# Kernel optimization log

Measured on AMD Instinct MI355X. Metric: run time of the kernel, lower is better.

## Reference

```python
import jax, jax.numpy as jnp
import numpy as np

N_NODES = 50000
N_EDGES = 600000
N_GRAPHS = 256
IN_C = 128
HID = 128
OUT_C = 2


def setup_inputs() -> dict:
    key = jax.random.key(0)
    ks = jax.random.split(key, 16)
    d = {}
    d["x"] = jax.random.normal(ks[0], (N_NODES, IN_C), jnp.float32)
    d["edge_index"] = jax.random.randint(ks[1], (2, N_EDGES), 0, N_NODES, dtype=jnp.int32)
    d["root_node_idx"] = jax.random.randint(ks[2], (N_GRAPHS,), 0, N_NODES, dtype=jnp.int32)
    d["batch"] = jnp.sort(jax.random.randint(ks[3], (N_NODES,), 0, N_GRAPHS, dtype=jnp.int32))
    dims = [(IN_C, HID), (HID, HID), (HID, HID), (HID, HID)]
    for i, (ci, co) in enumerate(dims, start=1):
        s = 1.0 / np.sqrt(ci)
        d[f"w{i}_l"] = jax.random.uniform(ks[3 + i], (co, ci), jnp.float32, -s, s)
        d[f"b{i}_l"] = jnp.zeros((co,), jnp.float32)
        d[f"w{i}_r"] = jax.random.uniform(ks[7 + i], (co, ci), jnp.float32, -s, s)
    s = 1.0 / np.sqrt(2 * HID)
    d["w_cls"] = jax.random.uniform(ks[12], (OUT_C, 2 * HID), jnp.float32, -s, s)
    d["b_cls"] = jnp.zeros((OUT_C,), jnp.float32)
    return d


def _sage_conv(x, src, tgt, deg_inv, w_l, b_l, w_r):
    # mean aggregation of source features at target nodes (PyG SAGEConv, aggr='mean')
    agg = jax.ops.segment_sum(x[src], tgt, num_segments=N_NODES) * deg_inv  # [N, C]
    # out = lin_l(agg) + lin_r(x); lin_r has no bias in PyG SAGEConv
    return agg @ w_l.T + b_l + x @ w_r.T


def reference(x, edge_index, root_node_idx, batch,
              w1_l, b1_l, w1_r, w2_l, b2_l, w2_r,
              w3_l, b3_l, w3_r, w4_l, b4_l, w4_r,
              w_cls, b_cls):
    src, tgt = edge_index[0], edge_index[1]
    ones_e = jnp.ones((src.shape[0],), x.dtype)
    deg = jax.ops.segment_sum(ones_e, tgt, num_segments=N_NODES)
    deg_inv = (1.0 / jnp.maximum(deg, 1.0))[:, None]  # [N, 1]

    h = jax.nn.relu(_sage_conv(x, src, tgt, deg_inv, w1_l, b1_l, w1_r))
    h = jax.nn.relu(_sage_conv(h, src, tgt, deg_inv, w2_l, b2_l, w2_r))
    h = jax.nn.relu(_sage_conv(h, src, tgt, deg_inv, w3_l, b3_l, w3_r))
    h = jax.nn.relu(_sage_conv(h, src, tgt, deg_inv, w4_l, b4_l, w4_r))

    root_emb = h[root_node_idx]  # [G, HID]
    g_sum = jax.ops.segment_sum(h, batch, num_segments=N_GRAPHS)
    g_cnt = jax.ops.segment_sum(jnp.ones((h.shape[0],), h.dtype), batch, num_segments=N_GRAPHS)
    graph_emb = g_sum / jnp.maximum(g_cnt, 1.0)[:, None]  # [G, HID]

    combined = jnp.concatenate([root_emb, graph_emb], axis=1)  # [G, 2*HID]
    return combined @ w_cls.T + b_cls  # [G, OUT_C]
```

## Files before the change

kernel.cpp:

```cpp
#include <hip/hip_runtime.h>
#include <hip/hip_bf16.h>

#define N_NODES 50000
#define N_EDGES 600000
#define N_GRAPHS 256
#define C 128
#define NB 196
#define PB_DEG 2344
#define PB_XS  6250
#define PB_WS  512

typedef unsigned short ushort;
typedef unsigned int uint;
typedef __attribute__((ext_vector_type(8))) short bfrag8;
typedef __attribute__((ext_vector_type(4))) float facc4;

__device__ __forceinline__ ushort f2bf(float v) {
    uint u = __float_as_uint(v);
    u += 0x7FFFu + ((u >> 16) & 1u);
    return (ushort)(u >> 16);
}
__device__ __forceinline__ float bf2f(ushort u) {
    return __uint_as_float(((uint)u) << 16);
}
__device__ __forceinline__ void fsplit(float v, ushort& h, ushort& l) {
    h = f2bf(v);
    l = f2bf(v - bf2f(h));
}

struct WPtrs { const float* wl[4]; const float* wr[4]; };

__global__ __launch_bounds__(256) void k_prep(const int* __restrict__ tgt,
                                              int* __restrict__ deg,
                                              const float* __restrict__ x,
                                              ushort* __restrict__ Ahi,
                                              ushort* __restrict__ Alo,
                                              WPtrs wp,
                                              ushort* __restrict__ BTh,
                                              ushort* __restrict__ BTl,
                                              const int* __restrict__ batch,
                                              int* __restrict__ gstart) {
    const int b = blockIdx.x, t = threadIdx.x;
    if (b < PB_DEG) {
        int e = b * 256 + t;
        if (e < N_EDGES) atomicAdd(&deg[tgt[e]], 1);
    } else if (b < PB_DEG + PB_XS) {
        int gid = (b - PB_DEG) * 256 + t;
        int n = gid >> 5, c4 = (gid & 31) << 2;
        float4 v = *(const float4*)(x + (size_t)n * C + c4);
        ushort4 h, l;
        fsplit(v.x, h.x, l.x); fsplit(v.y, h.y, l.y);
        fsplit(v.z, h.z, l.z); fsplit(v.w, h.w, l.w);
        *(ushort4*)(Ahi + (size_t)n * 256 + 128 + c4) = h;
        *(ushort4*)(Alo + (size_t)n * 256 + 128 + c4) = l;
    } else if (b < PB_DEG + PB_XS + PB_WS) {
        int gid = (b - PB_DEG - PB_XS) * 256 + t;
        int l = gid >> 15;
        int rem = gid & 32767;
        int n = rem >> 8, k = rem & 255;
        float v = (k < 128) ? wp.wl[l][n * 128 + k] : wp.wr[l][n * 128 + (k - 128)];
        ushort h, lo;
        fsplit(v, h, lo);
        BTh[gid] = h;
        BTl[gid] = lo;
    } else {
        int g = t;
        int lo = 0, hi = N_NODES;
        while (lo < hi) {
            int mid = (lo + hi) >> 1;
            if (batch[mid] < g) lo = mid + 1;
            else hi = mid;
        }
        gstart[g] = lo;
        if (t == 0) gstart[N_GRAPHS] = N_NODES;
    }
}

__global__ __launch_bounds__(256) void k_scan1(const int* __restrict__ deg,
                                               int* __restrict__ bsum,
                                               float* __restrict__ dinv) {
    __shared__ int ws[4];
    int idx = blockIdx.x * 256 + threadIdx.x;
    int v = (idx < N_NODES) ? deg[idx] : 0;
    if (idx < N_NODES) dinv[idx] = 1.0f / fmaxf((float)v, 1.0f);
    int s = v;
#pragma unroll
    for (int off = 1; off < 64; off <<= 1) s += __shfl_xor(s, off);
    if ((threadIdx.x & 63) == 0) ws[threadIdx.x >> 6] = s;
    __syncthreads();
    if (threadIdx.x == 0) bsum[blockIdx.x] = ws[0] + ws[1] + ws[2] + ws[3];
}

__global__ __launch_bounds__(256) void k_scan2(const int* __restrict__ deg,
                                               const int* __restrict__ bsum,
                                               int* __restrict__ rowptr) {
    __shared__ int red[4];
    __shared__ int ws[4];
    const int b = blockIdx.x, t = threadIdx.x;
    const int lane = t & 63, w = t >> 6;
    int bv = (t < NB && t < b) ? bsum[t] : 0;
#pragma unroll
    for (int off = 1; off < 64; off <<= 1) bv += __shfl_xor(bv, off);
    if (lane == 0) red[w] = bv;
    __syncthreads();
    const int boff = red[0] + red[1] + red[2] + red[3];
    int idx = b * 256 + t;
    int v = (idx < N_NODES) ? deg[idx] : 0;
    int incl = v;
#pragma unroll
    for (int off = 1; off < 64; off <<= 1) {
        int u = __shfl_up(incl, off);
        if (lane >= off) incl += u;
    }
    if (lane == 63) ws[w] = incl;
    __syncthreads();
    int wo = 0;
    if (w > 0) wo += ws[0];
    if (w > 1) wo += ws[1];
    if (w > 2) wo += ws[2];
    if (idx < N_NODES) rowptr[idx] = boff + wo + incl - v;
    if (b == 0 && t == 0) rowptr[N_NODES] = N_EDGES;
}

__global__ void k_fill(const int* __restrict__ src, const int* __restrict__ tgt,
                       const int* __restrict__ rowptr, int* __restrict__ fill,
                       int* __restrict__ csr_src) {
    int e = blockIdx.x * blockDim.x + threadIdx.x;
    if (e >= N_EDGES) return;
    int d = tgt[e];
    int pos = atomicAdd(&fill[d], 1);
    csr_src[rowptr[d] + pos] = src[e];
}

__global__ __launch_bounds__(256) void k_gather(const ushort* __restrict__ Ahi_r,
                                                const ushort* __restrict__ Alo_r,
                                                ushort* __restrict__ Ahi_w,
                                                ushort* __restrict__ Alo_w,
                                                const int* __restrict__ csr_src,
                                                const int* __restrict__ rowptr,
                                                const float* __restrict__ dinv) {
    int node = blockIdx.x * 8 + (threadIdx.x >> 5);
    if (node >= N_NODES) return;
    int lane = threadIdx.x & 31;
    int c4 = lane << 2;
    int s = rowptr[node], e = rowptr[node + 1];
    float sc = dinv[node];
    float a0 = 0.f, a1 = 0.f, a2 = 0.f, a3 = 0.f;
    int j = s;
    for (; j + 3 < e; j += 4) {
        int s0 = csr_src[j], s1 = csr_src[j + 1];
        int s2 = csr_src[j + 2], s3 = csr_src[j + 3];
        ushort4 h0 = *(const ushort4*)(Ahi_r + (size_t)s0 * 256 + 128 + c4);
        ushort4 l0 = *(const ushort4*)(Alo_r + (size_t)s0 * 256 + 128 + c4);
        ushort4 h1 = *(const ushort4*)(Ahi_r + (size_t)s1 * 256 + 128 + c4);
        ushort4 l1 = *(const ushort4*)(Alo_r + (size_t)s1 * 256 + 128 + c4);
        ushort4 h2 = *(const ushort4*)(Ahi_r + (size_t)s2 * 256 + 128 + c4);
        ushort4 l2 = *(const ushort4*)(Alo_r + (size_t)s2 * 256 + 128 + c4);
        ushort4 h3 = *(const ushort4*)(Ahi_r + (size_t)s3 * 256 + 128 + c4);
        ushort4 l3 = *(const ushort4*)(Alo_r + (size_t)s3 * 256 + 128 + c4);
        a0 += (bf2f(h0.x) + bf2f(l0.x)) + (bf2f(h1.x) + bf2f(l1.x))
            + (bf2f(h2.x) + bf2f(l2.x)) + (bf2f(h3.x) + bf2f(l3.x));
        a1 += (bf2f(h0.y) + bf2f(l0.y)) + (bf2f(h1.y) + bf2f(l1.y))
            + (bf2f(h2.y) + bf2f(l2.y)) + (bf2f(h3.y) + bf2f(l3.y));
        a2 += (bf2f(h0.z) + bf2f(l0.z)) + (bf2f(h1.z) + bf2f(l1.z))
            + (bf2f(h2.z) + bf2f(l2.z)) + (bf2f(h3.z) + bf2f(l3.z));
        a3 += (bf2f(h0.w) + bf2f(l0.w)) + (bf2f(h1.w) + bf2f(l1.w))
            + (bf2f(h2.w) + bf2f(l2.w)) + (bf2f(h3.w) + bf2f(l3.w));
    }
    for (; j < e; j++) {
        int s0 = csr_src[j];
        ushort4 h0 = *(const ushort4*)(Ahi_r + (size_t)s0 * 256 + 128 + c4);
        ushort4 l0 = *(const ushort4*)(Alo_r + (size_t)s0 * 256 + 128 + c4);
        a0 += bf2f(h0.x) + bf2f(l0.x);
        a1 += bf2f(h0.y) + bf2f(l0.y);
        a2 += bf2f(h0.z) + bf2f(l0.z);
        a3 += bf2f(h0.w) + bf2f(l0.w);
    }
    a0 *= sc; a1 *= sc; a2 *= sc; a3 *= sc;
    ushort4 h, l;
    fsplit(a0, h.x, l.x); fsplit(a1, h.y, l.y);
    fsplit(a2, h.z, l.z); fsplit(a3, h.w, l.w);
    *(ushort4*)(Ahi_w + (size_t)node * 256 + c4) = h;
    *(ushort4*)(Alo_w + (size_t)node * 256 + c4) = l;
}

__global__ __launch_bounds__(256) void k_gemm(const ushort* __restrict__ Ahi,
                                              const ushort* __restrict__ Alo,
                                              const ushort* __restrict__ BTh,
                                              const ushort* __restrict__ BTl,
                                              const float* __restrict__ bl,
                                              ushort* __restrict__ Hhi,
                                              ushort* __restrict__ Hlo) {
    __shared__ short As[2][128][40];
    __shared__ short Bs[2][128][40];
    const int tid = threadIdx.x;
    const int wave = tid >> 6, lane = tid & 63;
    const int m0 = blockIdx.x * 128;
    const int wm = (wave & 1) * 64;
    const int wn = (wave >> 1) * 64;
    const int l15 = lane & 15, lk = (lane >> 4) * 8;

    const int sr = tid >> 1;
    const int sc = (tid & 1) * 16;
    int garow = m0 + sr; if (garow >= N_NODES) garow = N_NODES - 1;
    const ushort* pAh = Ahi + (size_t)garow * 256 + sc;
    const ushort* pAl = Alo + (size_t)garow * 256 + sc;
    const ushort* pBh = BTh + sr * 256 + sc;
    const ushort* pBl = BTl + sr * 256 + sc;

    bfrag8 rAh0, rAh1, rAl0, rAl1, rBh0, rBh1, rBl0, rBl1;
#define LOADSTEP(K0) do { \
        rAh0 = *(const bfrag8*)(pAh + (K0));     rAh1 = *(const bfrag8*)(pAh + (K0) + 8); \
        rAl0 = *(const bfrag8*)(pAl + (K0));     rAl1 = *(const bfrag8*)(pAl + (K0) + 8); \
        rBh0 = *(const bfrag8*)(pBh + (K0));     rBh1 = *(const bfrag8*)(pBh + (K0) + 8); \
        rBl0 = *(const bfrag8*)(pBl + (K0));     rBl1 = *(const bfrag8*)(pBl + (K0) + 8); \
    } while (0)

    LOADSTEP(0);
    facc4 acc[4][4] = {};
#pragma unroll
    for (int s = 0; s < 8; s++) {
        *(bfrag8*)&As[0][sr][sc]     = rAh0;  *(bfrag8*)&As[0][sr][sc + 8] = rAh1;
        *(bfrag8*)&As[1][sr][sc]     = rAl0;  *(bfrag8*)&As[1][sr][sc + 8] = rAl1;
        *(bfrag8*)&Bs[0][sr][sc]     = rBh0;  *(bfrag8*)&Bs[0][sr][sc + 8] = rBh1;
        *(bfrag8*)&Bs[1][sr][sc]     = rBl0;  *(bfrag8*)&Bs[1][sr][sc + 8] = rBl1;
        __syncthreads();
        if (s < 7) LOADSTEP((s + 1) * 32);
        bfrag8 a[2][4], b[2][4];
#pragma unroll
        for (int t = 0; t < 4; t++) {
            a[0][t] = *(const bfrag8*)&As[0][wm + t * 16 + l15][lk];
            a[1][t] = *(const bfrag8*)&As[1][wm + t * 16 + l15][lk];
            b[0][t] = *(const bfrag8*)&Bs[0][wn + t * 16 + l15][lk];
            b[1][t] = *(const bfrag8*)&Bs[1][wn + t * 16 + l15][lk];
        }
#pragma unroll
        for (int mt = 0; mt < 4; mt++)
#pragma unroll
            for (int nt = 0; nt < 4; nt++) {
                acc[mt][nt] = __builtin_amdgcn_mfma_f32_16x16x32_bf16(a[0][mt], b[0][nt], acc[mt][nt], 0, 0, 0);
                acc[mt][nt] = __builtin_amdgcn_mfma_f32_16x16x32_bf16(a[0][mt], b[1][nt], acc[mt][nt], 0, 0, 0);
                acc[mt][nt] = __builtin_amdgcn_mfma_f32_16x16x32_bf16(a[1][mt], b[0][nt], acc[mt][nt], 0, 0, 0);
            }
        __syncthreads();
    }
#undef LOADSTEP

    const int r4 = (lane >> 4) * 4;
#pragma unroll
    for (int mt = 0; mt < 4; mt++) {
#pragma unroll
        for (int nt = 0; nt < 4; nt++) {
            int col = wn + nt * 16 + l15;
            float bias = bl[col];
#pragma unroll
            for (int r = 0; r < 4; r++) {
                int grow = m0 + wm + mt * 16 + r4 + r;
                if (grow < N_NODES) {
                    float v = fmaxf(acc[mt][nt][r] + bias, 0.f);
                    ushort h, l;
                    fsplit(v, h, l);
                    Hhi[(size_t)grow * 256 + 128 + col] = h;
                    Hlo[(size_t)grow * 256 + 128 + col] = l;
                }
            }
        }
    }
}

__global__ __launch_bounds__(256) void k_head(const ushort* __restrict__ Ahi,
                                              const ushort* __restrict__ Alo,
                                              const int* __restrict__ gstart,
                                              const int* __restrict__ root,
                                              const float* __restrict__ wcls,
                                              const float* __restrict__ bcls,
                                              float* __restrict__ out) {
    __shared__ float gm[128];
    __shared__ float part[128];
    __shared__ float red[8];
    const int g = blockIdx.x, t = threadIdx.x;
    const int c = t & 127, p = t >> 7;
    int s = gstart[g], e = gstart[g + 1];
    float sum = 0.f;
    for (int n = s + p; n < e; n += 2) {
        size_t o = (size_t)n * 256 + 128 + c;
        sum += bf2f(Ahi[o]) + bf2f(Alo[o]);
    }
    if (p) part[c] = sum;
    __syncthreads();
    if (!p) gm[c] = (sum + part[c]) / fmaxf((float)(e - s), 1.0f);
    __syncthreads();
    float v;
    if (t < 128) {
        size_t o = (size_t)root[g] * 256 + 128 + t;
        v = bf2f(Ahi[o]) + bf2f(Alo[o]);
    } else {
        v = gm[t - 128];
    }
    float p0 = v * wcls[t];
    float p1 = v * wcls[256 + t];
#pragma unroll
    for (int off = 32; off; off >>= 1) {
        p0 += __shfl_down(p0, off);
        p1 += __shfl_down(p1, off);
    }
    int wid = t >> 6;
    if ((t & 63) == 0) { red[wid] = p0; red[4 + wid] = p1; }
    __syncthreads();
    if (t == 0) {
        out[g * 2 + 0] = red[0] + red[1] + red[2] + red[3] + bcls[0];
        out[g * 2 + 1] = red[4] + red[5] + red[6] + red[7] + bcls[1];
    }
}

extern "C" void kernel_launch(void* const* d_in, const int* in_sizes, int n_in,
                              void* d_out, int out_size, void* d_ws, size_t ws_size,
                              hipStream_t stream) {
    const float* x = (const float*)d_in[0];
    const int* ei = (const int*)d_in[1];
    const int* src = ei;
    const int* tgt = ei + N_EDGES;
    const int* root = (const int*)d_in[2];
    const int* batch = (const int*)d_in[3];
    WPtrs wp;
    wp.wl[0] = (const float*)d_in[4];  wp.wr[0] = (const float*)d_in[6];
    wp.wl[1] = (const float*)d_in[7];  wp.wr[1] = (const float*)d_in[9];
    wp.wl[2] = (const float*)d_in[10]; wp.wr[2] = (const float*)d_in[12];
    wp.wl[3] = (const float*)d_in[13]; wp.wr[3] = (const float*)d_in[15];
    const float* blv[4] = {(const float*)d_in[5], (const float*)d_in[8],
                           (const float*)d_in[11], (const float*)d_in[14]};
    const float* wcls = (const float*)d_in[16];
    const float* bcls = (const float*)d_in[17];
    float* out = (float*)d_out;

    ushort* Ahi = (ushort*)d_ws;
    ushort* Alo = Ahi + (size_t)N_NODES * 256;
    ushort* BTh = Alo + (size_t)N_NODES * 256;
    ushort* BTl = BTh + 4 * 128 * 256;
    int* deg = (int*)(BTl + 4 * 128 * 256);
    int* fill = deg + N_NODES;
    float* dinv = (float*)(fill + N_NODES);
    int* rowptr = (int*)(dinv + N_NODES);
    int* csr_src = rowptr + N_NODES + 1;
    int* bsum = csr_src + N_EDGES;
    int* gstart = bsum + 256;

    hipMemsetAsync(deg, 0, 2 * N_NODES * sizeof(int), stream);
    k_prep<<<PB_DEG + PB_XS + PB_WS + 1, 256, 0, stream>>>(
        tgt, deg, x, Ahi, Alo, wp, BTh, BTl, batch, gstart);
    k_scan1<<<NB, 256, 0, stream>>>(deg, bsum, dinv);
    k_scan2<<<NB, 256, 0, stream>>>(deg, bsum, rowptr);
    k_fill<<<(N_EDGES + 255) / 256, 256, 0, stream>>>(src, tgt, rowptr, fill, csr_src);

    for (int l = 0; l < 4; l++) {
        k_gather<<<(N_NODES + 7) / 8, 256, 0, stream>>>(Ahi, Alo, Ahi, Alo,
                                                        csr_src, rowptr, dinv);
        k_gemm<<<(N_NODES + 127) / 128, 256, 0, stream>>>(
            Ahi, Alo, BTh + l * 32768, BTl + l * 32768, blv[l], Ahi, Alo);
    }
    k_head<<<N_GRAPHS, 256, 0, stream>>>(Ahi, Alo, gstart, root, wcls, bcls, out);
}
```

Measured before the change: 481.4 us.

## Store layer activations as fp32 and split to bf16 inside GEMM

Node activations are now kept as a compact fp32 [N,128] buffer instead of interleaved hi/lo bf16 halves in a 256-wide row. The gather kernel reads a single float4 per neighbour, and the GEMM splits the root-term fp32 values into hi/lo bf16 while staging them into shared memory. This removes the separate x split pass from the prep kernel, and the first layer reads x directly. In exchange the GEMM does extra conversion ALU work on half its K steps, and its output stores are fp32 scalar writes.

```diff
diff --git a/kernel.cpp b/kernel.cpp
--- a/kernel.cpp
+++ b/kernel.cpp
@@ -1,5 +1,4 @@
 #include <hip/hip_runtime.h>
-#include <hip/hip_bf16.h>
 
 #define N_NODES 50000
 #define N_EDGES 600000
@@ -7,7 +6,6 @@
 #define C 128
 #define NB 196
 #define PB_DEG 2344
-#define PB_XS  6250
 #define PB_WS  512
 
 typedef unsigned short ushort;
@@ -32,9 +30,6 @@
 
 __global__ __launch_bounds__(256) void k_prep(const int* __restrict__ tgt,
                                               int* __restrict__ deg,
-                                              const float* __restrict__ x,
-                                              ushort* __restrict__ Ahi,
-                                              ushort* __restrict__ Alo,
                                               WPtrs wp,
                                               ushort* __restrict__ BTh,
                                               ushort* __restrict__ BTl,
@@ -44,17 +39,8 @@
     if (b < PB_DEG) {
         int e = b * 256 + t;
         if (e < N_EDGES) atomicAdd(&deg[tgt[e]], 1);
-    } else if (b < PB_DEG + PB_XS) {
+    } else if (b < PB_DEG + PB_WS) {
         int gid = (b - PB_DEG) * 256 + t;
-        int n = gid >> 5, c4 = (gid & 31) << 2;
-        float4 v = *(const float4*)(x + (size_t)n * C + c4);
-        ushort4 h, l;
-        fsplit(v.x, h.x, l.x); fsplit(v.y, h.y, l.y);
-        fsplit(v.z, h.z, l.z); fsplit(v.w, h.w, l.w);
-        *(ushort4*)(Ahi + (size_t)n * 256 + 128 + c4) = h;
-        *(ushort4*)(Alo + (size_t)n * 256 + 128 + c4) = l;
-    } else if (b < PB_DEG + PB_XS + PB_WS) {
-        int gid = (b - PB_DEG - PB_XS) * 256 + t;
         int l = gid >> 15;
         int rem = gid & 32767;
         int n = rem >> 8, k = rem & 255;
@@ -132,10 +118,9 @@
     csr_src[rowptr[d] + pos] = src[e];
 }
 
-__global__ __launch_bounds__(256) void k_gather(const ushort* __restrict__ Ahi_r,
-                                                const ushort* __restrict__ Alo_r,
-                                                ushort* __restrict__ Ahi_w,
-                                                ushort* __restrict__ Alo_w,
+__global__ __launch_bounds__(256) void k_gather(const float* __restrict__ Hsrc,
+                                                ushort* __restrict__ AGhi,
+                                                ushort* __restrict__ AGlo,
                                                 const int* __restrict__ csr_src,
                                                 const int* __restrict__ rowptr,
                                                 const float* __restrict__ dinv) {
@@ -150,47 +135,35 @@
     for (; j + 3 < e; j += 4) {
         int s0 = csr_src[j], s1 = csr_src[j + 1];
         int s2 = csr_src[j + 2], s3 = csr_src[j + 3];
-        ushort4 h0 = *(const ushort4*)(Ahi_r + (size_t)s0 * 256 + 128 + c4);
-        ushort4 l0 = *(const ushort4*)(Alo_r + (size_t)s0 * 256 + 128 + c4);
-        ushort4 h1 = *(const ushort4*)(Ahi_r + (size_t)s1 * 256 + 128 + c4);
-        ushort4 l1 = *(const ushort4*)(Alo_r + (size_t)s1 * 256 + 128 + c4);
-        ushort4 h2 = *(const ushort4*)(Ahi_r + (size_t)s2 * 256 + 128 + c4);
-        ushort4 l2 = *(const ushort4*)(Alo_r + (size_t)s2 * 256 + 128 + c4);
-        ushort4 h3 = *(const ushort4*)(Ahi_r + (size_t)s3 * 256 + 128 + c4);
-        ushort4 l3 = *(const ushort4*)(Alo_r + (size_t)s3 * 256 + 128 + c4);
-        a0 += (bf2f(h0.x) + bf2f(l0.x)) + (bf2f(h1.x) + bf2f(l1.x))
-            + (bf2f(h2.x) + bf2f(l2.x)) + (bf2f(h3.x) + bf2f(l3.x));
-        a1 += (bf2f(h0.y) + bf2f(l0.y)) + (bf2f(h1.y) + bf2f(l1.y))
-            + (bf2f(h2.y) + bf2f(l2.y)) + (bf2f(h3.y) + bf2f(l3.y));
-        a2 += (bf2f(h0.z) + bf2f(l0.z)) + (bf2f(h1.z) + bf2f(l1.z))
-            + (bf2f(h2.z) + bf2f(l2.z)) + (bf2f(h3.z) + bf2f(l3.z));
-        a3 += (bf2f(h0.w) + bf2f(l0.w)) + (bf2f(h1.w) + bf2f(l1.w))
-            + (bf2f(h2.w) + bf2f(l2.w)) + (bf2f(h3.w) + bf2f(l3.w));
+        float4 v0 = *(const float4*)(Hsrc + (size_t)s0 * 128 + c4);
+        float4 v1 = *(const float4*)(Hsrc + (size_t)s1 * 128 + c4);
+        float4 v2 = *(const float4*)(Hsrc + (size_t)s2 * 128 + c4);
+        float4 v3 = *(const float4*)(Hsrc + (size_t)s3 * 128 + c4);
+        a0 += (v0.x + v1.x) + (v2.x + v3.x);
+        a1 += (v0.y + v1.y) + (v2.y + v3.y);
+        a2 += (v0.z + v1.z) + (v2.z + v3.z);
+        a3 += (v0.w + v1.w) + (v2.w + v3.w);
     }
     for (; j < e; j++) {
         int s0 = csr_src[j];
-        ushort4 h0 = *(const ushort4*)(Ahi_r + (size_t)s0 * 256 + 128 + c4);
-        ushort4 l0 = *(const ushort4*)(Alo_r + (size_t)s0 * 256 + 128 + c4);
-        a0 += bf2f(h0.x) + bf2f(l0.x);
-        a1 += bf2f(h0.y) + bf2f(l0.y);
-        a2 += bf2f(h0.z) + bf2f(l0.z);
-        a3 += bf2f(h0.w) + bf2f(l0.w);
+        float4 v0 = *(const float4*)(Hsrc + (size_t)s0 * 128 + c4);
+        a0 += v0.x; a1 += v0.y; a2 += v0.z; a3 += v0.w;
     }
     a0 *= sc; a1 *= sc; a2 *= sc; a3 *= sc;
     ushort4 h, l;
     fsplit(a0, h.x, l.x); fsplit(a1, h.y, l.y);
     fsplit(a2, h.z, l.z); fsplit(a3, h.w, l.w);
-    *(ushort4*)(Ahi_w + (size_t)node * 256 + c4) = h;
-    *(ushort4*)(Alo_w + (size_t)node * 256 + c4) = l;
-}
-
-__global__ __launch_bounds__(256) void k_gemm(const ushort* __restrict__ Ahi,
-                                              const ushort* __restrict__ Alo,
+    *(ushort4*)(AGhi + (size_t)node * 128 + c4) = h;
+    *(ushort4*)(AGlo + (size_t)node * 128 + c4) = l;
+}
+
+__global__ __launch_bounds__(256) void k_gemm(const ushort* __restrict__ AGhi,
+                                              const ushort* __restrict__ AGlo,
+                                              const float* __restrict__ Hsrc,
                                               const ushort* __restrict__ BTh,
                                               const ushort* __restrict__ BTl,
                                               const float* __restrict__ bl,
-                                              ushort* __restrict__ Hhi,
-                                              ushort* __restrict__ Hlo) {
+                                              float* __restrict__ Hout) {
     __shared__ short As[2][128][40];
     __shared__ short Bs[2][128][40];
     const int tid = threadIdx.x;
@@ -203,29 +176,52 @@
     const int sr = tid >> 1;
     const int sc = (tid & 1) * 16;
     int garow = m0 + sr; if (garow >= N_NODES) garow = N_NODES - 1;
-    const ushort* pAh = Ahi + (size_t)garow * 256 + sc;
-    const ushort* pAl = Alo + (size_t)garow * 256 + sc;
+    const ushort* pAh = AGhi + (size_t)garow * 128 + sc;
+    const ushort* pAl = AGlo + (size_t)garow * 128 + sc;
+    const float*  pHf = Hsrc + (size_t)garow * 128 + sc;
     const ushort* pBh = BTh + sr * 256 + sc;
     const ushort* pBl = BTl + sr * 256 + sc;
 
     bfrag8 rAh0, rAh1, rAl0, rAl1, rBh0, rBh1, rBl0, rBl1;
-#define LOADSTEP(K0) do { \
-        rAh0 = *(const bfrag8*)(pAh + (K0));     rAh1 = *(const bfrag8*)(pAh + (K0) + 8); \
-        rAl0 = *(const bfrag8*)(pAl + (K0));     rAl1 = *(const bfrag8*)(pAl + (K0) + 8); \
-        rBh0 = *(const bfrag8*)(pBh + (K0));     rBh1 = *(const bfrag8*)(pBh + (K0) + 8); \
-        rBl0 = *(const bfrag8*)(pBl + (K0));     rBl1 = *(const bfrag8*)(pBl + (K0) + 8); \
+    float4 f0, f1, f2, f3;
+#define LOADSTEP(S) do { \
+        if ((S) < 4) { \
+            rAh0 = *(const bfrag8*)(pAh + (S) * 32);     rAh1 = *(const bfrag8*)(pAh + (S) * 32 + 8); \
+            rAl0 = *(const bfrag8*)(pAl + (S) * 32);     rAl1 = *(const bfrag8*)(pAl + (S) * 32 + 8); \
+        } else { \
+            f0 = *(const float4*)(pHf + ((S) - 4) * 32);      f1 = *(const float4*)(pHf + ((S) - 4) * 32 + 4); \
+            f2 = *(const float4*)(pHf + ((S) - 4) * 32 + 8);  f3 = *(const float4*)(pHf + ((S) - 4) * 32 + 12); \
+        } \
+        rBh0 = *(const bfrag8*)(pBh + (S) * 32);     rBh1 = *(const bfrag8*)(pBh + (S) * 32 + 8); \
+        rBl0 = *(const bfrag8*)(pBl + (S) * 32);     rBl1 = *(const bfrag8*)(pBl + (S) * 32 + 8); \
     } while (0)
 
     LOADSTEP(0);
     facc4 acc[4][4] = {};
 #pragma unroll
     for (int s = 0; s < 8; s++) {
-        *(bfrag8*)&As[0][sr][sc]     = rAh0;  *(bfrag8*)&As[0][sr][sc + 8] = rAh1;
-        *(bfrag8*)&As[1][sr][sc]     = rAl0;  *(bfrag8*)&As[1][sr][sc + 8] = rAl1;
+        if (s < 4) {
+            *(bfrag8*)&As[0][sr][sc]     = rAh0;  *(bfrag8*)&As[0][sr][sc + 8] = rAh1;
+            *(bfrag8*)&As[1][sr][sc]     = rAl0;  *(bfrag8*)&As[1][sr][sc + 8] = rAl1;
+        } else {
+            float v[16] = {f0.x, f0.y, f0.z, f0.w, f1.x, f1.y, f1.z, f1.w,
+                           f2.x, f2.y, f2.z, f2.w, f3.x, f3.y, f3.z, f3.w};
+            ushort hh[16], ll[16];
+#pragma unroll
+            for (int i = 0; i < 16; i++) fsplit(v[i], hh[i], ll[i]);
+            bfrag8 H0, H1, L0, L1;
+#pragma unroll
+            for (int i = 0; i < 8; i++) {
+                H0[i] = (short)hh[i]; H1[i] = (short)hh[i + 8];
+                L0[i] = (short)ll[i]; L1[i] = (short)ll[i + 8];
+            }
+            *(bfrag8*)&As[0][sr][sc]     = H0;  *(bfrag8*)&As[0][sr][sc + 8] = H1;
+            *(bfrag8*)&As[1][sr][sc]     = L0;  *(bfrag8*)&As[1][sr][sc + 8] = L1;
+        }
         *(bfrag8*)&Bs[0][sr][sc]     = rBh0;  *(bfrag8*)&Bs[0][sr][sc + 8] = rBh1;
         *(bfrag8*)&Bs[1][sr][sc]     = rBl0;  *(bfrag8*)&Bs[1][sr][sc + 8] = rBl1;
         __syncthreads();
-        if (s < 7) LOADSTEP((s + 1) * 32);
+        if (s < 7) LOADSTEP(s + 1);
         bfrag8 a[2][4], b[2][4];
 #pragma unroll
         for (int t = 0; t < 4; t++) {
@@ -257,19 +253,14 @@
             for (int r = 0; r < 4; r++) {
                 int grow = m0 + wm + mt * 16 + r4 + r;
                 if (grow < N_NODES) {
-                    float v = fmaxf(acc[mt][nt][r] + bias, 0.f);
-                    ushort h, l;
-                    fsplit(v, h, l);
-                    Hhi[(size_t)grow * 256 + 128 + col] = h;
-                    Hlo[(size_t)grow * 256 + 128 + col] = l;
+                    Hout[(size_t)grow * 128 + col] = fmaxf(acc[mt][nt][r] + bias, 0.f);
                 }
             }
         }
     }
 }
 
-__global__ __launch_bounds__(256) void k_head(const ushort* __restrict__ Ahi,
-                                              const ushort* __restrict__ Alo,
+__global__ __launch_bounds__(256) void k_head(const float* __restrict__ H,
                                               const int* __restrict__ gstart,
                                               const int* __restrict__ root,
                                               const float* __restrict__ wcls,
@@ -283,8 +274,7 @@
     int s = gstart[g], e = gstart[g + 1];
     float sum = 0.f;
     for (int n = s + p; n < e; n += 2) {
-        size_t o = (size_t)n * 256 + 128 + c;
-        sum += bf2f(Ahi[o]) + bf2f(Alo[o]);
+        sum += H[(size_t)n * 128 + c];
     }
     if (p) part[c] = sum;
     __syncthreads();
@@ -292,8 +282,7 @@
     __syncthreads();
     float v;
     if (t < 128) {
-        size_t o = (size_t)root[g] * 256 + 128 + t;
-        v = bf2f(Ahi[o]) + bf2f(Alo[o]);
+        v = H[(size_t)root[g] * 128 + t];
     } else {
         v = gm[t - 128];
     }
@@ -333,9 +322,10 @@
     const float* bcls = (const float*)d_in[17];
     float* out = (float*)d_out;
 
-    ushort* Ahi = (ushort*)d_ws;
-    ushort* Alo = Ahi + (size_t)N_NODES * 256;
-    ushort* BTh = Alo + (size_t)N_NODES * 256;
+    float* H = (float*)d_ws;
+    ushort* AGhi = (ushort*)(H + (size_t)N_NODES * 128);
+    ushort* AGlo = AGhi + (size_t)N_NODES * 128;
+    ushort* BTh = AGlo + (size_t)N_NODES * 128;
     ushort* BTl = BTh + 4 * 128 * 256;
     int* deg = (int*)(BTl + 4 * 128 * 256);
     int* fill = deg + N_NODES;
@@ -346,17 +336,18 @@
     int* gstart = bsum + 256;
 
     hipMemsetAsync(deg, 0, 2 * N_NODES * sizeof(int), stream);
-    k_prep<<<PB_DEG + PB_XS + PB_WS + 1, 256, 0, stream>>>(
-        tgt, deg, x, Ahi, Alo, wp, BTh, BTl, batch, gstart);
+    k_prep<<<PB_DEG + PB_WS + 1, 256, 0, stream>>>(
+        tgt, deg, wp, BTh, BTl, batch, gstart);
     k_scan1<<<NB, 256, 0, stream>>>(deg, bsum, dinv);
     k_scan2<<<NB, 256, 0, stream>>>(deg, bsum, rowptr);
     k_fill<<<(N_EDGES + 255) / 256, 256, 0, stream>>>(src, tgt, rowptr, fill, csr_src);
 
     for (int l = 0; l < 4; l++) {
-        k_gather<<<(N_NODES + 7) / 8, 256, 0, stream>>>(Ahi, Alo, Ahi, Alo,
+        const float* hsrc = (l == 0) ? x : H;
+        k_gather<<<(N_NODES + 7) / 8, 256, 0, stream>>>(hsrc, AGhi, AGlo,
                                                         csr_src, rowptr, dinv);
         k_gemm<<<(N_NODES + 127) / 128, 256, 0, stream>>>(
-            Ahi, Alo, BTh + l * 32768, BTl + l * 32768, blv[l], Ahi, Alo);
-    }
-    k_head<<<N_GRAPHS, 256, 0, stream>>>(Ahi, Alo, gstart, root, wcls, bcls, out);
-}
+            AGhi, AGlo, hsrc, BTh + l * 32768, BTl + l * 32768, blv[l], H);
+    }
+    k_head<<<N_GRAPHS, 256, 0, stream>>>(H, gstart, root, wcls, bcls, out);
+}
```

Measured after the change: 459.7 us. -4.5%, faster.
